# Performance work log

Measured on AMD Instinct MI355X. Metric: run time of the kernel, lower is better.

The kernel has to match this reference:

```python
import jax, jax.numpy as jnp
import numpy as np

N_MODELS = 64
IN_F = 256
OUT_F = 256
BATCH = 8192


def setup_inputs() -> dict:
    key = jax.random.key(0)
    kx, kw, kb, ki = jax.random.split(key, 4)
    x = jax.random.normal(kx, (BATCH, OUT_F), dtype=jnp.float32)
    idxs = jax.random.randint(ki, (BATCH,), 0, N_MODELS, dtype=jnp.int64)
    # learned parameters (torch inits them to zeros; we use random so grads/outputs are nontrivial)
    w = jax.random.normal(kw, (N_MODELS, IN_F, OUT_F), dtype=jnp.float32) * 0.02
    b = jax.random.normal(kb, (N_MODELS, OUT_F), dtype=jnp.float32) * 0.02
    return {"x": x, "idxs": idxs, "w": w, "b": b}


def reference(x, idxs, w, b):
    # torch: baddbmm(b[idxs,:,None], w[idxs], x[:,:,None]).squeeze(-1) -> relu
    # y[n, i] = b[idxs[n], i] + sum_o w[idxs[n], i, o] * x[n, o]
    wg = w[idxs]                      # (B, in, out) gathered per-sample weights
    bg = b[idxs]                      # (B, out)
    y = jnp.einsum('bio,bo->bi', wg, x) + bg
    return jax.nn.relu(y)
```

## Files before the change

kernel.cpp:

```cpp
#include <hip/hip_runtime.h>
#include <stdint.h>


#define N_MODELS 64
#define IN_F     256
#define OUT_F    256
#define BATCH    8192
#define BM       128
#define BN       128
#define LP       40

typedef __bf16 bf16x8 __attribute__((ext_vector_type(8)));
typedef float  f32x4  __attribute__((ext_vector_type(4)));

__device__ __forceinline__ bf16x8 pack8(float4 a, float4 b) {
  bf16x8 o;
  o[0] = (__bf16)a.x; o[1] = (__bf16)a.y; o[2] = (__bf16)a.z; o[3] = (__bf16)a.w;
  o[4] = (__bf16)b.x; o[5] = (__bf16)b.y; o[6] = (__bf16)b.z; o[7] = (__bf16)b.w;
  return o;
}

__global__ __launch_bounds__(256) void fused_kernel(
    const float* __restrict__ x, const int* __restrict__ idxs,
    const float* __restrict__ w, const float* __restrict__ bias_g,
    float* __restrict__ out) {
  const int model = blockIdx.x >> 2;
  const int tile  = (blockIdx.x >> 1) & 1;
  const int i0    = (blockIdx.x & 1) * BN;
  const int t     = threadIdx.x;
  const int lane  = t & 63;
  const int wv    = t >> 6;

  __shared__ unsigned short a_lds[2][BM][LP];
  __shared__ unsigned short b_lds[2][BN][LP];
  __shared__ int rid[BM];
  __shared__ int wsum[4];

  const int r = t >> 1;
  const int h = t & 1;

  const float* wrow = w + (size_t)model * IN_F * OUT_F + (size_t)(i0 + r) * IN_F + h * 16;
  float4 rb[2][4];
#pragma unroll
  for (int j = 0; j < 4; ++j) rb[0][j] = *(const float4*)(wrow + j * 4);

  const int wm   = (wv & 1) * 64;
  const int wn   = (wv >> 1) * 64;
  const int col  = lane & 15;
  const int quad = lane >> 4;
  float bv[4];
  const float* bp = bias_g + model * OUT_F + i0 + wn + col;
#pragma unroll
  for (int nt = 0; nt < 4; ++nt) bv[nt] = bp[nt * 16];

  if (t < BM) rid[t] = -1;

  const int4* ip = (const int4*)idxs + t * 8;
  int cnt = 0;
#pragma unroll
  for (int j = 0; j < 8; ++j) {
    int4 v = ip[j];
    cnt += (v.x == model) + (v.y == model) + (v.z == model) + (v.w == model);
  }
  int inc = cnt;
#pragma unroll
  for (int d = 1; d < 64; d <<= 1) {
    int u = __shfl_up(inc, d);
    if (lane >= d) inc += u;
  }
  if (lane == 63) wsum[wv] = inc;
  __syncthreads();
  int wpre = 0, total = 0;
#pragma unroll
  for (int j = 0; j < 4; ++j) {
    int s = wsum[j];
    total += s;
    if (j < wv) wpre += s;
  }
  const int start = tile * BM;
  if (start >= total) return;

  int off = wpre + inc - cnt - start;
#pragma unroll
  for (int j = 0; j < 8; ++j) {
    int4 v = ip[j];
    int n0 = t * 32 + j * 4;
    if (v.x == model) { if ((unsigned)off < BM) rid[off] = n0 + 0; ++off; }
    if (v.y == model) { if ((unsigned)off < BM) rid[off] = n0 + 1; ++off; }
    if (v.z == model) { if ((unsigned)off < BM) rid[off] = n0 + 2; ++off; }
    if (v.w == model) { if ((unsigned)off < BM) rid[off] = n0 + 3; ++off; }
  }
  __syncthreads();

  const int srow = rid[r];
  const float* xrow = x + (size_t)(srow < 0 ? 0 : srow) * IN_F + h * 16;

  float4 ra[2][4];
#pragma unroll
  for (int j = 0; j < 4; ++j) ra[0][j] = *(const float4*)(xrow + j * 4);

  f32x4 acc[4][4];
#pragma unroll
  for (int mt = 0; mt < 4; ++mt)
#pragma unroll
    for (int nt = 0; nt < 4; ++nt)
      acc[mt][nt] = (f32x4){bv[nt], bv[nt], bv[nt], bv[nt]};

#pragma unroll
  for (int it = 0; it < 8; ++it) {
    const int cur = it & 1;
    if (it < 7) {
      const int kn = (it + 1) * 32;
#pragma unroll
      for (int j = 0; j < 4; ++j) {
        ra[cur ^ 1][j] = *(const float4*)(xrow + kn + j * 4);
        rb[cur ^ 1][j] = *(const float4*)(wrow + kn + j * 4);
      }
    }
    *(bf16x8*)&a_lds[cur][r][h * 16] = pack8(ra[cur][0], ra[cur][1]);
    *(bf16x8*)&a_lds[cur][r][h * 16 + 8] = pack8(ra[cur][2], ra[cur][3]);
    *(bf16x8*)&b_lds[cur][r][h * 16] = pack8(rb[cur][0], rb[cur][1]);
    *(bf16x8*)&b_lds[cur][r][h * 16 + 8] = pack8(rb[cur][2], rb[cur][3]);
    __syncthreads();

    bf16x8 af[4], bfr[4];
#pragma unroll
    for (int mt = 0; mt < 4; ++mt)
      af[mt] = *(const bf16x8*)&a_lds[cur][wm + mt * 16 + col][quad * 8];
#pragma unroll
    for (int nt = 0; nt < 4; ++nt)
      bfr[nt] = *(const bf16x8*)&b_lds[cur][wn + nt * 16 + col][quad * 8];
#pragma unroll
    for (int mt = 0; mt < 4; ++mt)
#pragma unroll
      for (int nt = 0; nt < 4; ++nt)
        acc[mt][nt] = __builtin_amdgcn_mfma_f32_16x16x32_bf16(
            af[mt], bfr[nt], acc[mt][nt], 0, 0, 0);
  }

#pragma unroll
  for (int mt = 0; mt < 4; ++mt) {
#pragma unroll
    for (int reg = 0; reg < 4; ++reg) {
      const int mm = wm + mt * 16 + quad * 4 + reg;
      const int s = rid[mm];
      if (s >= 0) {
        float* orow = out + (size_t)s * OUT_F + i0 + wn + col;
#pragma unroll
        for (int nt = 0; nt < 4; ++nt)
          orow[nt * 16] = fmaxf(acc[mt][nt][reg], 0.0f);
      }
    }
  }
}

extern "C" void kernel_launch(void* const* d_in, const int* in_sizes, int n_in,
                              void* d_out, int out_size, void* d_ws, size_t ws_size,
                              hipStream_t stream) {
  const float* x    = (const float*)d_in[0];
  const int*   idxs = (const int*)d_in[1];
  const float* w    = (const float*)d_in[2];
  const float* b    = (const float*)d_in[3];
  float* out = (float*)d_out;
  (void)d_ws; (void)ws_size;

  fused_kernel<<<N_MODELS * 4, 256, 0, stream>>>(x, idxs, w, b, out);
}
```

Before: 86.72 us.

## Stage full K extent in LDS once instead of double-buffered K-loop

Replaces the 8-step double-buffered K loop with a single bulk load of the whole 256-wide K dimension for both the x tile and the weight tile into padded LDS (264 stride), followed by one barrier and an MFMA loop that reads only from LDS. For tile 0 the weight load is issued before the index scan so it overlaps the routing phase, and the idx vector is read once into registers and reused. This removes per-iteration barriers and serial load/convert/sync stalls but raises LDS use to about 135KB per block, which cuts occupancy and removes overlap of global loads with MFMA in the main loop.

New measurement: 88.72 us. 1.02x slower.

```diff
diff --git a/kernel.cpp b/kernel.cpp
--- a/kernel.cpp
+++ b/kernel.cpp
@@ -8,7 +8,7 @@
 #define BATCH    8192
 #define BM       128
 #define BN       128
-#define LP       40
+#define PK       264
 
 typedef __bf16 bf16x8 __attribute__((ext_vector_type(8)));
 typedef float  f32x4  __attribute__((ext_vector_type(4)));
@@ -31,35 +31,36 @@
   const int lane  = t & 63;
   const int wv    = t >> 6;
 
-  __shared__ unsigned short a_lds[2][BM][LP];
-  __shared__ unsigned short b_lds[2][BN][LP];
+  __shared__ unsigned short a_lds[BM][PK];
+  __shared__ unsigned short b_lds[BN][PK];
   __shared__ int rid[BM];
   __shared__ int wsum[4];
 
-  const int r = t >> 1;
-  const int h = t & 1;
+  const int rw = t >> 1;
+  const int h  = t & 1;
 
-  const float* wrow = w + (size_t)model * IN_F * OUT_F + (size_t)(i0 + r) * IN_F + h * 16;
-  float4 rb[2][4];
+  const int4* ip = (const int4*)idxs + t * 8;
+  int4 iv[8];
 #pragma unroll
-  for (int j = 0; j < 4; ++j) rb[0][j] = *(const float4*)(wrow + j * 4);
+  for (int j = 0; j < 8; ++j) iv[j] = ip[j];
 
-  const int wm   = (wv & 1) * 64;
-  const int wn   = (wv >> 1) * 64;
-  const int col  = lane & 15;
-  const int quad = lane >> 4;
-  float bv[4];
-  const float* bp = bias_g + model * OUT_F + i0 + wn + col;
+  const float* wrow = w + (size_t)model * (IN_F * OUT_F)
+                        + (size_t)(i0 + rw) * IN_F + h * 128;
+  if (tile == 0) {
 #pragma unroll
-  for (int nt = 0; nt < 4; ++nt) bv[nt] = bp[nt * 16];
+    for (int j = 0; j < 16; ++j) {
+      float4 a = *(const float4*)(wrow + j * 8);
+      float4 b = *(const float4*)(wrow + j * 8 + 4);
+      *(bf16x8*)&b_lds[rw][h * 128 + j * 8] = pack8(a, b);
+    }
+  }
 
   if (t < BM) rid[t] = -1;
 
-  const int4* ip = (const int4*)idxs + t * 8;
   int cnt = 0;
 #pragma unroll
   for (int j = 0; j < 8; ++j) {
-    int4 v = ip[j];
+    int4 v = iv[j];
     cnt += (v.x == model) + (v.y == model) + (v.z == model) + (v.w == model);
   }
   int inc = cnt;
@@ -79,11 +80,10 @@
   }
   const int start = tile * BM;
   if (start >= total) return;
-
   int off = wpre + inc - cnt - start;
 #pragma unroll
   for (int j = 0; j < 8; ++j) {
-    int4 v = ip[j];
+    int4 v = iv[j];
     int n0 = t * 32 + j * 4;
     if (v.x == model) { if ((unsigned)off < BM) rid[off] = n0 + 0; ++off; }
     if (v.y == model) { if ((unsigned)off < BM) rid[off] = n0 + 1; ++off; }
@@ -92,12 +92,34 @@
   }
   __syncthreads();
 
-  const int srow = rid[r];
-  const float* xrow = x + (size_t)(srow < 0 ? 0 : srow) * IN_F + h * 16;
+  if (tile == 1) {
+#pragma unroll
+    for (int j = 0; j < 16; ++j) {
+      float4 a = *(const float4*)(wrow + j * 8);
+      float4 b = *(const float4*)(wrow + j * 8 + 4);
+      *(bf16x8*)&b_lds[rw][h * 128 + j * 8] = pack8(a, b);
+    }
+  }
 
-  float4 ra[2][4];
+  const int srow = rid[rw];
+  const float* xrow = x + (size_t)(srow < 0 ? 0 : srow) * IN_F + h * 128;
 #pragma unroll
-  for (int j = 0; j < 4; ++j) ra[0][j] = *(const float4*)(xrow + j * 4);
+  for (int j = 0; j < 16; ++j) {
+    float4 a = *(const float4*)(xrow + j * 8);
+    float4 b = *(const float4*)(xrow + j * 8 + 4);
+    *(bf16x8*)&a_lds[rw][h * 128 + j * 8] = pack8(a, b);
+  }
+
+  const int wm   = (wv & 1) * 64;
+  const int wn   = (wv >> 1) * 64;
+  const int col  = lane & 15;
+  const int quad = lane >> 4;
+  float bv[4];
+  const float* bp = bias_g + model * OUT_F + i0 + wn + col;
+#pragma unroll
+  for (int nt = 0; nt < 4; ++nt) bv[nt] = bp[nt * 16];
+
+  __syncthreads();
 
   f32x4 acc[4][4];
 #pragma unroll
@@ -107,29 +129,14 @@
       acc[mt][nt] = (f32x4){bv[nt], bv[nt], bv[nt], bv[nt]};
 
 #pragma unroll
-  for (int it = 0; it < 8; ++it) {
-    const int cur = it & 1;
-    if (it < 7) {
-      const int kn = (it + 1) * 32;
-#pragma unroll
-      for (int j = 0; j < 4; ++j) {
-        ra[cur ^ 1][j] = *(const float4*)(xrow + kn + j * 4);
-        rb[cur ^ 1][j] = *(const float4*)(wrow + kn + j * 4);
-      }
-    }
-    *(bf16x8*)&a_lds[cur][r][h * 16] = pack8(ra[cur][0], ra[cur][1]);
-    *(bf16x8*)&a_lds[cur][r][h * 16 + 8] = pack8(ra[cur][2], ra[cur][3]);
-    *(bf16x8*)&b_lds[cur][r][h * 16] = pack8(rb[cur][0], rb[cur][1]);
-    *(bf16x8*)&b_lds[cur][r][h * 16 + 8] = pack8(rb[cur][2], rb[cur][3]);
-    __syncthreads();
-
+  for (int ks = 0; ks < 8; ++ks) {
     bf16x8 af[4], bfr[4];
 #pragma unroll
     for (int mt = 0; mt < 4; ++mt)
-      af[mt] = *(const bf16x8*)&a_lds[cur][wm + mt * 16 + col][quad * 8];
+      af[mt] = *(const bf16x8*)&a_lds[wm + mt * 16 + col][ks * 32 + quad * 8];
 #pragma unroll
     for (int nt = 0; nt < 4; ++nt)
-      bfr[nt] = *(const bf16x8*)&b_lds[cur][wn + nt * 16 + col][quad * 8];
+      bfr[nt] = *(const bf16x8*)&b_lds[wn + nt * 16 + col][ks * 32 + quad * 8];
 #pragma unroll
     for (int mt = 0; mt < 4; ++mt)
 #pragma unroll
```
